# Kernel optimization log

Hardware: AMD Instinct MI355X
Metric: run time of the kernel (lower is better)

Reference implementation:

```python
import jax, jax.numpy as jnp
import numpy as np

D_MODEL = 1024
NUM_HEADS = 16
HEAD_DIM = D_MODEL // NUM_HEADS
THETA = 10000.0
B, S = 4, 2048


def _rope(x, pos):
    # x: [B, H, S, d], pos: [B, S] int
    half = HEAD_DIM // 2
    inv_freq = THETA ** (-(jnp.arange(half, dtype=jnp.float32) * 2.0) / HEAD_DIM)  # [half]
    ang = pos.astype(jnp.float32)[:, None, :, None] * inv_freq  # [B, 1, S, half]
    cos, sin = jnp.cos(ang), jnp.sin(ang)
    x1, x2 = x[..., 0::2], x[..., 1::2]  # interleaved pairs
    r1 = x1 * cos - x2 * sin
    r2 = x1 * sin + x2 * cos
    return jnp.stack([r1, r2], axis=-1).reshape(x.shape)


def setup_inputs() -> dict:
    key = jax.random.key(0)
    ks = jax.random.split(key, 12)
    scale = 1.0 / np.sqrt(D_MODEL)
    inp = {
        "query": jax.random.normal(ks[0], (B, S, D_MODEL), dtype=jnp.float32),
        "key": jax.random.normal(ks[1], (B, S, D_MODEL), dtype=jnp.float32),
        "value": jax.random.normal(ks[2], (B, S, D_MODEL), dtype=jnp.float32),
        "token_positions": jnp.broadcast_to(jnp.arange(S, dtype=jnp.int32), (B, S)),
        "w_q": jax.random.normal(ks[3], (D_MODEL, D_MODEL), dtype=jnp.float32) * scale,
        "b_q": jnp.zeros((D_MODEL,), dtype=jnp.float32),
        "w_k": jax.random.normal(ks[4], (D_MODEL, D_MODEL), dtype=jnp.float32) * scale,
        "b_k": jnp.zeros((D_MODEL,), dtype=jnp.float32),
        "w_v": jax.random.normal(ks[5], (D_MODEL, D_MODEL), dtype=jnp.float32) * scale,
        "b_v": jnp.zeros((D_MODEL,), dtype=jnp.float32),
        "w_o": jax.random.normal(ks[6], (D_MODEL, D_MODEL), dtype=jnp.float32) * scale,
        "b_o": jnp.zeros((D_MODEL,), dtype=jnp.float32),
    }
    return inp


def reference(query, key, value, token_positions, w_q, b_q, w_k, b_k, w_v, b_v, w_o, b_o):
    b, s, _ = query.shape
    Q = query @ w_q + b_q
    K = key @ w_k + b_k
    V = value @ w_v + b_v
    # [B, S, H, d] -> [B, H, S, d]
    Q = Q.reshape(b, s, NUM_HEADS, HEAD_DIM).transpose(0, 2, 1, 3)
    K = K.reshape(b, s, NUM_HEADS, HEAD_DIM).transpose(0, 2, 1, 3)
    V = V.reshape(b, s, NUM_HEADS, HEAD_DIM).transpose(0, 2, 1, 3)
    Q = _rope(Q, token_positions)
    K = _rope(K, token_positions)
    scores = jnp.einsum("bhqd,bhkd->bhqk", Q, K) / jnp.sqrt(jnp.float32(HEAD_DIM))
    causal = jnp.tril(jnp.ones((s, s), dtype=bool))
    scores = jnp.where(causal, scores, -jnp.inf)
    attn = jax.nn.softmax(scores, axis=-1)
    out = jnp.einsum("bhqk,bhkd->bhqd", attn, V)
    out = out.transpose(0, 2, 1, 3).reshape(b, s, D_MODEL)
    return out @ w_o + b_o
```

## Files before the change

kernel.cpp:

```cpp
#include <hip/hip_runtime.h>

typedef __bf16 bf16;
typedef __attribute__((ext_vector_type(8))) __bf16 bf16x8;
typedef __attribute__((ext_vector_type(4))) __bf16 bf16x4;
typedef __attribute__((ext_vector_type(4))) float floatx4;

#define MFMA16(a, b, c) __builtin_amdgcn_mfma_f32_16x16x32_bf16((a), (b), (c), 0, 0, 0)

#define GLL(g, l)                                                   \
  __builtin_amdgcn_global_load_lds(                                 \
      (const __attribute__((address_space(1))) void*)(g),           \
      (__attribute__((address_space(3))) void*)(l), 16, 0, 0)

static constexpr int DM = 1024;
static constexpr int SEQ = 2048;
static constexpr int BATCH = 4;
static constexpr int NH = 16;
static constexpr int HD = 64;
static constexpr float LOG2E = 1.4426950408889634f;
static constexpr float LOG2_THETA = 13.287712379549449f;
static constexpr float QSC = 0.125f * LOG2E;

__global__ __launch_bounds__(256) void convert_x(
    const float* __restrict__ q, const float* __restrict__ k,
    const float* __restrict__ v, bf16* __restrict__ qo,
    bf16* __restrict__ ko, bf16* __restrict__ vo) {
  int z = blockIdx.z;
  const float* src = (z == 0) ? q : (z == 1) ? k : v;
  bf16* dst = (z == 0) ? qo : (z == 1) ? ko : vo;
  size_t i = ((size_t)blockIdx.x * blockDim.x + threadIdx.x) * 8;
  float4 a = *(const float4*)(src + i);
  float4 b = *(const float4*)(src + i + 4);
  bf16x8 o;
  o[0] = (bf16)a.x; o[1] = (bf16)a.y; o[2] = (bf16)a.z; o[3] = (bf16)a.w;
  o[4] = (bf16)b.x; o[5] = (bf16)b.y; o[6] = (bf16)b.z; o[7] = (bf16)b.w;
  *(bf16x8*)(dst + i) = o;
}

__global__ __launch_bounds__(256) void convert_w(
    const float* __restrict__ wq, const float* __restrict__ wk,
    const float* __restrict__ wv, const float* __restrict__ wo,
    bf16* __restrict__ oq, bf16* __restrict__ ok, bf16* __restrict__ ov,
    bf16* __restrict__ oo) {
  int z = blockIdx.z;
  const float* src = (z == 0) ? wq : (z == 1) ? wk : (z == 2) ? wv : wo;
  bf16* dst = (z == 0) ? oq : (z == 1) ? ok : (z == 2) ? ov : oo;
  __shared__ __align__(16) bf16 T[64][72];
  int k0 = blockIdx.y * 64, n0 = blockIdx.x * 64;
  int tid = threadIdx.x;
  int r = tid >> 4, c4 = (tid & 15) * 4;
#pragma unroll
  for (int i = 0; i < 4; i++) {
    int kk = r + i * 16;
    float4 v = *(const float4*)(src + (size_t)(k0 + kk) * DM + n0 + c4);
    T[c4 + 0][kk] = (bf16)v.x;
    T[c4 + 1][kk] = (bf16)v.y;
    T[c4 + 2][kk] = (bf16)v.z;
    T[c4 + 3][kk] = (bf16)v.w;
  }
  __syncthreads();
#pragma unroll
  for (int i = 0; i < 4; i++) {
    int nn = r + i * 16;
    bf16x4 o = *(const bf16x4*)&T[nn][c4];
    *(bf16x4*)(dst + (size_t)(n0 + nn) * DM + k0 + c4) = o;
  }
}

__global__ __launch_bounds__(256) void rope_table(const int* __restrict__ tp,
                                                  float* __restrict__ tab) {
  int idx = blockIdx.x * 256 + threadIdx.x;
  int m = idx >> 5, i = idx & 31;
  float pos = (float)tp[m];
  float invf = exp2f(-(float)(2 * i) * (LOG2_THETA / 64.0f));
  float s, c;
  sincosf(pos * invf, &s, &c);
  tab[(size_t)idx * 2] = c;
  tab[(size_t)idx * 2 + 1] = s;
}

__global__ __launch_bounds__(256) void gemm_qkv(
    const bf16* __restrict__ qb, const bf16* __restrict__ kb,
    const bf16* __restrict__ vb, const bf16* __restrict__ wqt,
    const bf16* __restrict__ wkt, const bf16* __restrict__ wvt,
    const float* __restrict__ biq, const float* __restrict__ bik,
    const float* __restrict__ biv, const float* __restrict__ tab,
    bf16* __restrict__ Qr, bf16* __restrict__ Kr, bf16* __restrict__ Vr) {
  int z = blockIdx.z;
  const bf16* X = (z == 0) ? qb : (z == 1) ? kb : vb;
  const bf16* Wt = (z == 0) ? wqt : (z == 1) ? wkt : wvt;
  const float* bias = (z == 0) ? biq : (z == 1) ? bik : biv;

  __shared__ __align__(16) bf16 As[128 * 32];
  __shared__ __align__(16) bf16 Bs[128 * 32];
  int lin = blockIdx.x;
  int m0 = (lin & 63) * 128, n0 = (lin >> 6) * 128;
  int tid = threadIdx.x;
  int lane = tid & 63, wv = tid >> 6;
  int quad = lane >> 4, low = lane & 15;
  int wm = (wv >> 1) * 64, wn = (wv & 1) * 64;
  int lr = lane >> 2, lc = (lane & 3) * 8;
  const bf16* AgL = X + (size_t)(m0 + wv * 16 + lr) * DM + lc;
  const bf16* BgL = Wt + (size_t)(n0 + wv * 16 + lr) * DM + lc;
  bf16* AsL = As + wv * 512;
  bf16* BsL = Bs + wv * 512;

  floatx4 acc[4][4];
#pragma unroll
  for (int i = 0; i < 4; i++)
#pragma unroll
    for (int j = 0; j < 4; j++) acc[i][j] = (floatx4)0.0f;

  for (int kt = 0; kt < DM; kt += 32) {
    GLL(AgL + kt, AsL);
    GLL(AgL + kt + (size_t)64 * DM, AsL + 2048);
    GLL(BgL + kt, BsL);
    GLL(BgL + kt + (size_t)64 * DM, BsL + 2048);
    __syncthreads();
    bf16x8 xf[4], wf[4];
#pragma unroll
    for (int t = 0; t < 4; t++)
      xf[t] = *(const bf16x8*)&As[(wm + t * 16 + low) * 32 + quad * 8];
#pragma unroll
    for (int t = 0; t < 4; t++)
      wf[t] = *(const bf16x8*)&Bs[(wn + t * 16 + low) * 32 + quad * 8];
#pragma unroll
    for (int i = 0; i < 4; i++)
#pragma unroll
      for (int j = 0; j < 4; j++)
        acc[i][j] = MFMA16(wf[i], xf[j], acc[i][j]);
    __syncthreads();
  }

#pragma unroll
  for (int i = 0; i < 4; i++) {
    int nb = n0 + wn + i * 16 + quad * 4;
    float4 bv = *(const float4*)(bias + nb);
    int h = nb >> 6, dbase = nb & 63;
#pragma unroll
    for (int j = 0; j < 4; j++) {
      int m = m0 + wm + j * 16 + low;
      int bb = m >> 11, ss = m & 2047;
      float v0 = acc[i][j][0] + bv.x;
      float v1 = acc[i][j][1] + bv.y;
      float v2 = acc[i][j][2] + bv.z;
      float v3 = acc[i][j][3] + bv.w;
      size_t off = ((size_t)(bb * NH + h) * SEQ + ss) * HD + dbase;
      bf16x4 pk;
      if (z < 2) {
        float4 cs = *(const float4*)(tab + (size_t)m * 64 + dbase);
        float o0 = v0 * cs.x - v1 * cs.y;
        float o1 = v0 * cs.y + v1 * cs.x;
        float o2 = v2 * cs.z - v3 * cs.w;
        float o3 = v2 * cs.w + v3 * cs.z;
        if (z == 0) { o0 *= QSC; o1 *= QSC; o2 *= QSC; o3 *= QSC; }
        pk[0] = (bf16)o0; pk[1] = (bf16)o1;
        pk[2] = (bf16)o2; pk[3] = (bf16)o3;
        bf16* dst = (z == 0) ? Qr : Kr;
        *(bf16x4*)(dst + off) = pk;
      } else {
        pk[0] = (bf16)v0; pk[1] = (bf16)v1;
        pk[2] = (bf16)v2; pk[3] = (bf16)v3;
        *(bf16x4*)(Vr + off) = pk;
      }
    }
  }
}

__global__ __launch_bounds__(256) void transpose_v(const bf16* __restrict__ Vr,
                                                   bf16* __restrict__ Vt) {
  int bh = blockIdx.y;
  int s0 = blockIdx.x * 64;
  __shared__ __align__(16) bf16 T[64][72];
  int t = threadIdx.x;
  int r = t >> 2, c = (t & 3) * 16;
  const bf16* src = Vr + ((size_t)bh * SEQ + s0 + r) * HD + c;
  bf16x8 a = *(const bf16x8*)src;
  bf16x8 b = *(const bf16x8*)(src + 8);
  *(bf16x8*)&T[r][c] = a;
  *(bf16x8*)&T[r][c + 8] = b;
  __syncthreads();
  bf16* dst = Vt + ((size_t)bh * HD + r) * SEQ + s0 + c;
  bf16x8 o0, o1;
#pragma unroll
  for (int j = 0; j < 8; j++) {
    o0[j] = T[c + j][r];
    o1[j] = T[c + 8 + j][r];
  }
  *(bf16x8*)dst = o0;
  *(bf16x8*)(dst + 8) = o1;
}

__global__ __launch_bounds__(256, 2) void attn_fa(const bf16* __restrict__ Qr,
                                                  const bf16* __restrict__ Kr,
                                                  const bf16* __restrict__ Vt,
                                                  bf16* __restrict__ attn) {
  int lin = blockIdx.x;
  int bh = lin & 63, bx = lin >> 6;
  int tid = threadIdx.x, lane = tid & 63, w = tid >> 6;
  int quad = lane >> 4, low = lane & 15;
  __shared__ __align__(16) bf16 Ks[2][64 * 72];
  __shared__ __align__(16) bf16 Vs[2][64 * 72];
  __shared__ __align__(16) bf16 Pl[4][2][16 * 72];
  const bf16* Qh = Qr + (size_t)bh * SEQ * HD;
  const bf16* Kh = Kr + (size_t)bh * SEQ * HD;
  const bf16* Vh = Vt + (size_t)bh * HD * SEQ;
  int bb = bh >> 4, h = bh & 15;

  int sr = tid >> 2, scol = (tid & 3) * 16;
  const bf16* Kg = Kh + (size_t)sr * HD + scol;
  const bf16* Vg = Vh + (size_t)sr * SEQ + scol;
  int sl = sr * 72 + scol;

  bf16x8 ones;
#pragma unroll
  for (int j = 0; j < 8; j++) ones[j] = (bf16)1.0f;

  for (int pass = 0; pass < 2; pass++) {
    int qi = pass ? bx : (15 - bx);
    int ntiles = 2 * qi + 2;
    int qrow0 = qi * 128 + w * 32;

    bf16x8 aq[2][2];
#pragma unroll
    for (int rt = 0; rt < 2; rt++)
#pragma unroll
      for (int kc = 0; kc < 2; kc++)
        aq[rt][kc] = *(const bf16x8*)(Qh +
                                      (size_t)(qrow0 + rt * 16 + low) * HD +
                                      kc * 32 + quad * 8);

    floatx4 accO[2][4];
    floatx4 lacc[2];
#pragma unroll
    for (int rt = 0; rt < 2; rt++) {
      lacc[rt] = (floatx4)0.0f;
#pragma unroll
      for (int nt = 0; nt < 4; nt++) accO[rt][nt] = (floatx4)0.0f;
    }

    {
      bf16x8 k0 = *(const bf16x8*)(Kg);
      bf16x8 k1 = *(const bf16x8*)(Kg + 8);
      bf16x8 v0 = *(const bf16x8*)(Vg);
      bf16x8 v1 = *(const bf16x8*)(Vg + 8);
      *(bf16x8*)&Ks[0][sl] = k0;
      *(bf16x8*)&Ks[0][sl + 8] = k1;
      *(bf16x8*)&Vs[0][sl] = v0;
      *(bf16x8*)&Vs[0][sl + 8] = v1;
    }
    __syncthreads();

    for (int kt = 0; kt < ntiles; kt++) {
      int cur = kt & 1;
      bf16x8 nk0, nk1, nv0, nv1;
      bool pre = (kt + 1 < ntiles);
      if (pre) {
        const bf16* kg = Kg + (size_t)(kt + 1) * (64 * HD);
        const bf16* vg = Vg + (size_t)(kt + 1) * 64;
        nk0 = *(const bf16x8*)(kg);
        nk1 = *(const bf16x8*)(kg + 8);
        nv0 = *(const bf16x8*)(vg);
        nv1 = *(const bf16x8*)(vg + 8);
      }

      floatx4 s2[2][4];
#pragma unroll
      for (int rt = 0; rt < 2; rt++)
#pragma unroll
        for (int nt = 0; nt < 4; nt++) s2[rt][nt] = (floatx4)0.0f;
#pragma unroll
      for (int nt = 0; nt < 4; nt++) {
        bf16x8 kb0 = *(const bf16x8*)&Ks[cur][(nt * 16 + low) * 72 + quad * 8];
        bf16x8 kb1 =
            *(const bf16x8*)&Ks[cur][(nt * 16 + low) * 72 + 32 + quad * 8];
#pragma unroll
        for (int rt = 0; rt < 2; rt++) {
          s2[rt][nt] = MFMA16(kb0, aq[rt][0], s2[rt][nt]);
          s2[rt][nt] = MFMA16(kb1, aq[rt][1], s2[rt][nt]);
        }
      }
      if (kt >= ntiles - 2) {
#pragma unroll
        for (int nt = 0; nt < 4; nt++)
#pragma unroll
          for (int r = 0; r < 4; r++) {
            int kg_ = kt * 64 + nt * 16 + quad * 4 + r;
#pragma unroll
            for (int rt = 0; rt < 2; rt++) {
              int qg = qrow0 + rt * 16 + low;
              if (kg_ > qg) s2[rt][nt][r] = -INFINITY;
            }
          }
      }
#pragma unroll
      for (int rt = 0; rt < 2; rt++)
#pragma unroll
        for (int nt = 0; nt < 4; nt++) {
          bf16x4 pk;
#pragma unroll
          for (int r = 0; r < 4; r++) pk[r] = (bf16)exp2f(s2[rt][nt][r]);
          *(bf16x4*)&Pl[w][rt][low * 72 + nt * 16 + quad * 4] = pk;
        }
      bf16x8 vb0[4], vb1[4];
#pragma unroll
      for (int nt = 0; nt < 4; nt++) {
        vb0[nt] = *(const bf16x8*)&Vs[cur][(nt * 16 + low) * 72 + quad * 8];
        vb1[nt] =
            *(const bf16x8*)&Vs[cur][(nt * 16 + low) * 72 + 32 + quad * 8];
      }
      asm volatile("s_waitcnt lgkmcnt(0)" ::: "memory");
#pragma unroll
      for (int rt = 0; rt < 2; rt++) {
        bf16x8 ap0 = *(const bf16x8*)&Pl[w][rt][low * 72 + quad * 8];
        bf16x8 ap1 = *(const bf16x8*)&Pl[w][rt][low * 72 + 32 + quad * 8];
#pragma unroll
        for (int nt = 0; nt < 4; nt++) {
          accO[rt][nt] = MFMA16(ap0, vb0[nt], accO[rt][nt]);
          accO[rt][nt] = MFMA16(ap1, vb1[nt], accO[rt][nt]);
        }
        lacc[rt] = MFMA16(ap0, ones, lacc[rt]);
        lacc[rt] = MFMA16(ap1, ones, lacc[rt]);
      }
      if (pre) {
        int nb = cur ^ 1;
        *(bf16x8*)&Ks[nb][sl] = nk0;
        *(bf16x8*)&Ks[nb][sl + 8] = nk1;
        *(bf16x8*)&Vs[nb][sl] = nv0;
        *(bf16x8*)&Vs[nb][sl + 8] = nv1;
      }
      __syncthreads();
    }

#pragma unroll
    for (int rt = 0; rt < 2; rt++)
#pragma unroll
      for (int r = 0; r < 4; r++) {
        float inv = 1.0f / lacc[rt][r];
        int q = qrow0 + rt * 16 + quad * 4 + r;
#pragma unroll
        for (int nt = 0; nt < 4; nt++) {
          float o = accO[rt][nt][r] * inv;
          attn[((size_t)(bb * SEQ + q)) * DM + h * HD + nt * 16 + low] =
              (bf16)o;
        }
      }
  }
}

__global__ __launch_bounds__(256) void gemm_out(const bf16* __restrict__ X,
                                                const bf16* __restrict__ Wt,
                                                const float* __restrict__ bias,
                                                float* __restrict__ out) {
  __shared__ __align__(16) bf16 As[128 * 32];
  __shared__ __align__(16) bf16 Bs[128 * 32];
  int lin = blockIdx.x;
  int m0 = (lin & 63) * 128, n0 = (lin >> 6) * 128;
  int tid = threadIdx.x;
  int lane = tid & 63, wv = tid >> 6;
  int quad = lane >> 4, low = lane & 15;
  int wm = (wv >> 1) * 64, wn = (wv & 1) * 64;
  int lr = lane >> 2, lc = (lane & 3) * 8;
  const bf16* AgL = X + (size_t)(m0 + wv * 16 + lr) * DM + lc;
  const bf16* BgL = Wt + (size_t)(n0 + wv * 16 + lr) * DM + lc;
  bf16* AsL = As + wv * 512;
  bf16* BsL = Bs + wv * 512;

  floatx4 acc[4][4];
#pragma unroll
  for (int i = 0; i < 4; i++)
#pragma unroll
    for (int j = 0; j < 4; j++) acc[i][j] = (floatx4)0.0f;

  for (int kt = 0; kt < DM; kt += 32) {
    GLL(AgL + kt, AsL);
    GLL(AgL + kt + (size_t)64 * DM, AsL + 2048);
    GLL(BgL + kt, BsL);
    GLL(BgL + kt + (size_t)64 * DM, BsL + 2048);
    __syncthreads();
    bf16x8 xf[4], wf[4];
#pragma unroll
    for (int t = 0; t < 4; t++)
      xf[t] = *(const bf16x8*)&As[(wm + t * 16 + low) * 32 + quad * 8];
#pragma unroll
    for (int t = 0; t < 4; t++)
      wf[t] = *(const bf16x8*)&Bs[(wn + t * 16 + low) * 32 + quad * 8];
#pragma unroll
    for (int i = 0; i < 4; i++)
#pragma unroll
      for (int j = 0; j < 4; j++)
        acc[i][j] = MFMA16(wf[i], xf[j], acc[i][j]);
    __syncthreads();
  }

#pragma unroll
  for (int i = 0; i < 4; i++) {
    int nb = n0 + wn + i * 16 + quad * 4;
    float4 bv = *(const float4*)(bias + nb);
#pragma unroll
    for (int j = 0; j < 4; j++) {
      int m = m0 + wm + j * 16 + low;
      float4 o;
      o.x = acc[i][j][0] + bv.x;
      o.y = acc[i][j][1] + bv.y;
      o.z = acc[i][j][2] + bv.z;
      o.w = acc[i][j][3] + bv.w;
      *(float4*)(out + (size_t)m * DM + nb) = o;
    }
  }
}

extern "C" void kernel_launch(void* const* d_in, const int* in_sizes, int n_in,
                              void* d_out, int out_size, void* d_ws,
                              size_t ws_size, hipStream_t stream) {
  const float* query = (const float*)d_in[0];
  const float* key_ = (const float*)d_in[1];
  const float* value = (const float*)d_in[2];
  const int* tp = (const int*)d_in[3];
  const float* w_q = (const float*)d_in[4];
  const float* b_q = (const float*)d_in[5];
  const float* w_k = (const float*)d_in[6];
  const float* b_k = (const float*)d_in[7];
  const float* w_v = (const float*)d_in[8];
  const float* b_v = (const float*)d_in[9];
  const float* w_o = (const float*)d_in[10];
  const float* b_o = (const float*)d_in[11];

  char* w = (char*)d_ws;
  const size_t MB = 1u << 20;
  bf16* qb = (bf16*)(w + 0);
  bf16* kb = (bf16*)(w + 16 * MB);
  bf16* vb = (bf16*)(w + 32 * MB);
  bf16* wqt = (bf16*)(w + 48 * MB);
  bf16* wkt = (bf16*)(w + 50 * MB);
  bf16* wvt = (bf16*)(w + 52 * MB);
  bf16* wot = (bf16*)(w + 54 * MB);
  bf16* Qr = (bf16*)(w + 56 * MB);
  bf16* Kr = (bf16*)(w + 72 * MB);
  bf16* Vr = (bf16*)(w + 88 * MB);
  float* tab = (float*)(w + 104 * MB);
  bf16* Vt = (bf16*)(w + 32 * MB);
  bf16* attnb = (bf16*)(w + 0);

  convert_x<<<dim3(4096, 1, 3), 256, 0, stream>>>(query, key_, value, qb, kb,
                                                  vb);
  convert_w<<<dim3(16, 16, 4), 256, 0, stream>>>(w_q, w_k, w_v, w_o, wqt, wkt,
                                                 wvt, wot);
  rope_table<<<1024, 256, 0, stream>>>(tp, tab);
  gemm_qkv<<<dim3(512, 1, 3), 256, 0, stream>>>(qb, kb, vb, wqt, wkt, wvt,
                                                b_q, b_k, b_v, tab, Qr, Kr,
                                                Vr);
  transpose_v<<<dim3(32, 64), 256, 0, stream>>>(Vr, Vt);
  attn_fa<<<dim3(512), 256, 0, stream>>>(Qr, Kr, Vt, attnb);
  gemm_out<<<dim3(512), 256, 0, stream>>>(attnb, wot, b_o, (float*)d_out);
}
```

Baseline: 353.5 us.

## Widen GEMM K-tile with XOR-swizzled LDS and split attention into one tile per block

Both projection GEMMs now stage a 64-wide K slice per iteration into LDS using an XOR swizzle on the column chunk. This halves the number of barriers per K loop and is meant to avoid LDS bank conflicts on the fragment reads. The attention kernel drops the two-pass pairing of query tiles and launches 1024 blocks, each handling one query tile. It also uses a single P staging buffer per wave and raises the occupancy hint to 3 blocks per CU. The balanced pairing that evened out causal work is lost in favour of more, smaller blocks and higher occupancy.

Result: faster. 334.0 us (-5.5%).

```diff
diff --git a/kernel.cpp b/kernel.cpp
--- a/kernel.cpp
+++ b/kernel.cpp
@@ -91,19 +91,21 @@
   const bf16* Wt = (z == 0) ? wqt : (z == 1) ? wkt : wvt;
   const float* bias = (z == 0) ? biq : (z == 1) ? bik : biv;
 
-  __shared__ __align__(16) bf16 As[128 * 32];
-  __shared__ __align__(16) bf16 Bs[128 * 32];
+  __shared__ __align__(16) bf16 As[128 * 64];
+  __shared__ __align__(16) bf16 Bs[128 * 64];
   int lin = blockIdx.x;
   int m0 = (lin & 63) * 128, n0 = (lin >> 6) * 128;
   int tid = threadIdx.x;
   int lane = tid & 63, wv = tid >> 6;
   int quad = lane >> 4, low = lane & 15;
   int wm = (wv >> 1) * 64, wn = (wv & 1) * 64;
-  int lr = lane >> 2, lc = (lane & 3) * 8;
-  const bf16* AgL = X + (size_t)(m0 + wv * 16 + lr) * DM + lc;
-  const bf16* BgL = Wt + (size_t)(n0 + wv * 16 + lr) * DM + lc;
-  bf16* AsL = As + wv * 512;
-  bf16* BsL = Bs + wv * 512;
+  int lr8 = lane >> 3;
+  int swcol = ((lane & 7) ^ lr8) * 8;
+  const bf16* AgL = X + (size_t)(m0 + wv * 8 + lr8) * DM + swcol;
+  const bf16* BgL = Wt + (size_t)(n0 + wv * 8 + lr8) * DM + swcol;
+  bf16* AsL = As + wv * 8 * 64;
+  bf16* BsL = Bs + wv * 8 * 64;
+  int r3 = low & 7;
 
   floatx4 acc[4][4];
 #pragma unroll
@@ -111,24 +113,30 @@
 #pragma unroll
     for (int j = 0; j < 4; j++) acc[i][j] = (floatx4)0.0f;
 
-  for (int kt = 0; kt < DM; kt += 32) {
-    GLL(AgL + kt, AsL);
-    GLL(AgL + kt + (size_t)64 * DM, AsL + 2048);
-    GLL(BgL + kt, BsL);
-    GLL(BgL + kt + (size_t)64 * DM, BsL + 2048);
+  for (int kt = 0; kt < DM; kt += 64) {
+#pragma unroll
+    for (int c = 0; c < 4; c++) {
+      GLL(AgL + kt + (size_t)(c * 32) * DM, AsL + c * 2048);
+      GLL(BgL + kt + (size_t)(c * 32) * DM, BsL + c * 2048);
+    }
     __syncthreads();
-    bf16x8 xf[4], wf[4];
-#pragma unroll
-    for (int t = 0; t < 4; t++)
-      xf[t] = *(const bf16x8*)&As[(wm + t * 16 + low) * 32 + quad * 8];
-#pragma unroll
-    for (int t = 0; t < 4; t++)
-      wf[t] = *(const bf16x8*)&Bs[(wn + t * 16 + low) * 32 + quad * 8];
-#pragma unroll
-    for (int i = 0; i < 4; i++)
-#pragma unroll
-      for (int j = 0; j < 4; j++)
-        acc[i][j] = MFMA16(wf[i], xf[j], acc[i][j]);
+#pragma unroll
+    for (int kc = 0; kc < 2; kc++) {
+      bf16x8 xf[4], wf[4];
+#pragma unroll
+      for (int t = 0; t < 4; t++)
+        xf[t] = *(const bf16x8*)&As[(wm + t * 16 + low) * 64 +
+                                    (((kc << 2) | quad) ^ r3) * 8];
+#pragma unroll
+      for (int t = 0; t < 4; t++)
+        wf[t] = *(const bf16x8*)&Bs[(wn + t * 16 + low) * 64 +
+                                    (((kc << 2) | quad) ^ r3) * 8];
+#pragma unroll
+      for (int i = 0; i < 4; i++)
+#pragma unroll
+        for (int j = 0; j < 4; j++)
+          acc[i][j] = MFMA16(wf[i], xf[j], acc[i][j]);
+    }
     __syncthreads();
   }
 
@@ -191,21 +199,23 @@
   *(bf16x8*)(dst + 8) = o1;
 }
 
-__global__ __launch_bounds__(256, 2) void attn_fa(const bf16* __restrict__ Qr,
+__global__ __launch_bounds__(256, 3) void attn_fa(const bf16* __restrict__ Qr,
                                                   const bf16* __restrict__ Kr,
                                                   const bf16* __restrict__ Vt,
                                                   bf16* __restrict__ attn) {
   int lin = blockIdx.x;
-  int bh = lin & 63, bx = lin >> 6;
+  int bh = lin & 63, qi = 15 - (lin >> 6);
+  int ntiles = 2 * qi + 2;
   int tid = threadIdx.x, lane = tid & 63, w = tid >> 6;
   int quad = lane >> 4, low = lane & 15;
   __shared__ __align__(16) bf16 Ks[2][64 * 72];
   __shared__ __align__(16) bf16 Vs[2][64 * 72];
-  __shared__ __align__(16) bf16 Pl[4][2][16 * 72];
+  __shared__ __align__(16) bf16 Pl[4][16 * 72];
   const bf16* Qh = Qr + (size_t)bh * SEQ * HD;
   const bf16* Kh = Kr + (size_t)bh * SEQ * HD;
   const bf16* Vh = Vt + (size_t)bh * HD * SEQ;
   int bb = bh >> 4, h = bh & 15;
+  int qrow0 = qi * 128 + w * 32;
 
   int sr = tid >> 2, scol = (tid & 3) * 16;
   const bf16* Kg = Kh + (size_t)sr * HD + scol;
@@ -216,155 +226,150 @@
 #pragma unroll
   for (int j = 0; j < 8; j++) ones[j] = (bf16)1.0f;
 
-  for (int pass = 0; pass < 2; pass++) {
-    int qi = pass ? bx : (15 - bx);
-    int ntiles = 2 * qi + 2;
-    int qrow0 = qi * 128 + w * 32;
-
-    bf16x8 aq[2][2];
+  bf16x8 aq[2][2];
+#pragma unroll
+  for (int rt = 0; rt < 2; rt++)
+#pragma unroll
+    for (int kc = 0; kc < 2; kc++)
+      aq[rt][kc] = *(const bf16x8*)(Qh + (size_t)(qrow0 + rt * 16 + low) * HD +
+                                    kc * 32 + quad * 8);
+
+  floatx4 accO[2][4];
+  floatx4 lacc[2];
+#pragma unroll
+  for (int rt = 0; rt < 2; rt++) {
+    lacc[rt] = (floatx4)0.0f;
+#pragma unroll
+    for (int nt = 0; nt < 4; nt++) accO[rt][nt] = (floatx4)0.0f;
+  }
+
+  {
+    bf16x8 k0 = *(const bf16x8*)(Kg);
+    bf16x8 k1 = *(const bf16x8*)(Kg + 8);
+    bf16x8 v0 = *(const bf16x8*)(Vg);
+    bf16x8 v1 = *(const bf16x8*)(Vg + 8);
+    *(bf16x8*)&Ks[0][sl] = k0;
+    *(bf16x8*)&Ks[0][sl + 8] = k1;
+    *(bf16x8*)&Vs[0][sl] = v0;
+    *(bf16x8*)&Vs[0][sl + 8] = v1;
+  }
+  __syncthreads();
+
+  for (int kt = 0; kt < ntiles; kt++) {
+    int cur = kt & 1;
+    bf16x8 nk0, nk1, nv0, nv1;
+    bool pre = (kt + 1 < ntiles);
+    if (pre) {
+      const bf16* kg = Kg + (size_t)(kt + 1) * (64 * HD);
+      const bf16* vg = Vg + (size_t)(kt + 1) * 64;
+      nk0 = *(const bf16x8*)(kg);
+      nk1 = *(const bf16x8*)(kg + 8);
+      nv0 = *(const bf16x8*)(vg);
+      nv1 = *(const bf16x8*)(vg + 8);
+    }
+
+    floatx4 s2[2][4];
 #pragma unroll
     for (int rt = 0; rt < 2; rt++)
 #pragma unroll
-      for (int kc = 0; kc < 2; kc++)
-        aq[rt][kc] = *(const bf16x8*)(Qh +
-                                      (size_t)(qrow0 + rt * 16 + low) * HD +
-                                      kc * 32 + quad * 8);
-
-    floatx4 accO[2][4];
-    floatx4 lacc[2];
+      for (int nt = 0; nt < 4; nt++) s2[rt][nt] = (floatx4)0.0f;
+#pragma unroll
+    for (int nt = 0; nt < 4; nt++) {
+      bf16x8 kb0 = *(const bf16x8*)&Ks[cur][(nt * 16 + low) * 72 + quad * 8];
+      bf16x8 kb1 =
+          *(const bf16x8*)&Ks[cur][(nt * 16 + low) * 72 + 32 + quad * 8];
+#pragma unroll
+      for (int rt = 0; rt < 2; rt++) {
+        s2[rt][nt] = MFMA16(kb0, aq[rt][0], s2[rt][nt]);
+        s2[rt][nt] = MFMA16(kb1, aq[rt][1], s2[rt][nt]);
+      }
+    }
+    if (kt >= ntiles - 2) {
+#pragma unroll
+      for (int nt = 0; nt < 4; nt++)
+#pragma unroll
+        for (int r = 0; r < 4; r++) {
+          int kg_ = kt * 64 + nt * 16 + quad * 4 + r;
+#pragma unroll
+          for (int rt = 0; rt < 2; rt++) {
+            int qg = qrow0 + rt * 16 + low;
+            if (kg_ > qg) s2[rt][nt][r] = -INFINITY;
+          }
+        }
+    }
+    bf16x4 pk[2][4];
+#pragma unroll
+    for (int rt = 0; rt < 2; rt++)
+#pragma unroll
+      for (int nt = 0; nt < 4; nt++)
+#pragma unroll
+        for (int r = 0; r < 4; r++)
+          pk[rt][nt][r] = (bf16)exp2f(s2[rt][nt][r]);
+    bf16x8 vb0[4], vb1[4];
+#pragma unroll
+    for (int nt = 0; nt < 4; nt++) {
+      vb0[nt] = *(const bf16x8*)&Vs[cur][(nt * 16 + low) * 72 + quad * 8];
+      vb1[nt] = *(const bf16x8*)&Vs[cur][(nt * 16 + low) * 72 + 32 + quad * 8];
+    }
 #pragma unroll
     for (int rt = 0; rt < 2; rt++) {
-      lacc[rt] = (floatx4)0.0f;
-#pragma unroll
-      for (int nt = 0; nt < 4; nt++) accO[rt][nt] = (floatx4)0.0f;
-    }
-
-    {
-      bf16x8 k0 = *(const bf16x8*)(Kg);
-      bf16x8 k1 = *(const bf16x8*)(Kg + 8);
-      bf16x8 v0 = *(const bf16x8*)(Vg);
-      bf16x8 v1 = *(const bf16x8*)(Vg + 8);
-      *(bf16x8*)&Ks[0][sl] = k0;
-      *(bf16x8*)&Ks[0][sl + 8] = k1;
-      *(bf16x8*)&Vs[0][sl] = v0;
-      *(bf16x8*)&Vs[0][sl + 8] = v1;
+#pragma unroll
+      for (int nt = 0; nt < 4; nt++)
+        *(bf16x4*)&Pl[w][low * 72 + nt * 16 + quad * 4] = pk[rt][nt];
+      asm volatile("s_waitcnt lgkmcnt(0)" ::: "memory");
+      bf16x8 ap0 = *(const bf16x8*)&Pl[w][low * 72 + quad * 8];
+      bf16x8 ap1 = *(const bf16x8*)&Pl[w][low * 72 + 32 + quad * 8];
+#pragma unroll
+      for (int nt = 0; nt < 4; nt++) {
+        accO[rt][nt] = MFMA16(ap0, vb0[nt], accO[rt][nt]);
+        accO[rt][nt] = MFMA16(ap1, vb1[nt], accO[rt][nt]);
+      }
+      lacc[rt] = MFMA16(ap0, ones, lacc[rt]);
+      lacc[rt] = MFMA16(ap1, ones, lacc[rt]);
+    }
+    if (pre) {
+      int nb = cur ^ 1;
+      *(bf16x8*)&Ks[nb][sl] = nk0;
+      *(bf16x8*)&Ks[nb][sl + 8] = nk1;
+      *(bf16x8*)&Vs[nb][sl] = nv0;
+      *(bf16x8*)&Vs[nb][sl + 8] = nv1;
     }
     __syncthreads();
-
-    for (int kt = 0; kt < ntiles; kt++) {
-      int cur = kt & 1;
-      bf16x8 nk0, nk1, nv0, nv1;
-      bool pre = (kt + 1 < ntiles);
-      if (pre) {
-        const bf16* kg = Kg + (size_t)(kt + 1) * (64 * HD);
-        const bf16* vg = Vg + (size_t)(kt + 1) * 64;
-        nk0 = *(const bf16x8*)(kg);
-        nk1 = *(const bf16x8*)(kg + 8);
-        nv0 = *(const bf16x8*)(vg);
-        nv1 = *(const bf16x8*)(vg + 8);
+  }
+
+#pragma unroll
+  for (int rt = 0; rt < 2; rt++)
+#pragma unroll
+    for (int r = 0; r < 4; r++) {
+      float inv = 1.0f / lacc[rt][r];
+      int q = qrow0 + rt * 16 + quad * 4 + r;
+#pragma unroll
+      for (int nt = 0; nt < 4; nt++) {
+        float o = accO[rt][nt][r] * inv;
+        attn[((size_t)(bb * SEQ + q)) * DM + h * HD + nt * 16 + low] = (bf16)o;
       }
-
-      floatx4 s2[2][4];
-#pragma unroll
-      for (int rt = 0; rt < 2; rt++)
-#pragma unroll
-        for (int nt = 0; nt < 4; nt++) s2[rt][nt] = (floatx4)0.0f;
-#pragma unroll
-      for (int nt = 0; nt < 4; nt++) {
-        bf16x8 kb0 = *(const bf16x8*)&Ks[cur][(nt * 16 + low) * 72 + quad * 8];
-        bf16x8 kb1 =
-            *(const bf16x8*)&Ks[cur][(nt * 16 + low) * 72 + 32 + quad * 8];
-#pragma unroll
-        for (int rt = 0; rt < 2; rt++) {
-          s2[rt][nt] = MFMA16(kb0, aq[rt][0], s2[rt][nt]);
-          s2[rt][nt] = MFMA16(kb1, aq[rt][1], s2[rt][nt]);
-        }
-      }
-      if (kt >= ntiles - 2) {
-#pragma unroll
-        for (int nt = 0; nt < 4; nt++)
-#pragma unroll
-          for (int r = 0; r < 4; r++) {
-            int kg_ = kt * 64 + nt * 16 + quad * 4 + r;
-#pragma unroll
-            for (int rt = 0; rt < 2; rt++) {
-              int qg = qrow0 + rt * 16 + low;
-              if (kg_ > qg) s2[rt][nt][r] = -INFINITY;
-            }
-          }
-      }
-#pragma unroll
-      for (int rt = 0; rt < 2; rt++)
-#pragma unroll
-        for (int nt = 0; nt < 4; nt++) {
-          bf16x4 pk;
-#pragma unroll
-          for (int r = 0; r < 4; r++) pk[r] = (bf16)exp2f(s2[rt][nt][r]);
-          *(bf16x4*)&Pl[w][rt][low * 72 + nt * 16 + quad * 4] = pk;
-        }
-      bf16x8 vb0[4], vb1[4];
-#pragma unroll
-      for (int nt = 0; nt < 4; nt++) {
-        vb0[nt] = *(const bf16x8*)&Vs[cur][(nt * 16 + low) * 72 + quad * 8];
-        vb1[nt] =
-            *(const bf16x8*)&Vs[cur][(nt * 16 + low) * 72 + 32 + quad * 8];
-      }
-      asm volatile("s_waitcnt lgkmcnt(0)" ::: "memory");
-#pragma unroll
-      for (int rt = 0; rt < 2; rt++) {
-        bf16x8 ap0 = *(const bf16x8*)&Pl[w][rt][low * 72 + quad * 8];
-        bf16x8 ap1 = *(const bf16x8*)&Pl[w][rt][low * 72 + 32 + quad * 8];
-#pragma unroll
-        for (int nt = 0; nt < 4; nt++) {
-          accO[rt][nt] = MFMA16(ap0, vb0[nt], accO[rt][nt]);
-          accO[rt][nt] = MFMA16(ap1, vb1[nt], accO[rt][nt]);
-        }
-        lacc[rt] = MFMA16(ap0, ones, lacc[rt]);
-        lacc[rt] = MFMA16(ap1, ones, lacc[rt]);
-      }
-      if (pre) {
-        int nb = cur ^ 1;
-        *(bf16x8*)&Ks[nb][sl] = nk0;
-        *(bf16x8*)&Ks[nb][sl + 8] = nk1;
-        *(bf16x8*)&Vs[nb][sl] = nv0;
-        *(bf16x8*)&Vs[nb][sl + 8] = nv1;
-      }
-      __syncthreads();
-    }
-
-#pragma unroll
-    for (int rt = 0; rt < 2; rt++)
-#pragma unroll
-      for (int r = 0; r < 4; r++) {
-        float inv = 1.0f / lacc[rt][r];
-        int q = qrow0 + rt * 16 + quad * 4 + r;
-#pragma unroll
-        for (int nt = 0; nt < 4; nt++) {
-          float o = accO[rt][nt][r] * inv;
-          attn[((size_t)(bb * SEQ + q)) * DM + h * HD + nt * 16 + low] =
-              (bf16)o;
-        }
-      }
-  }
+    }
 }
 
 __global__ __launch_bounds__(256) void gemm_out(const bf16* __restrict__ X,
                                                 const bf16* __restrict__ Wt,
                                                 const float* __restrict__ bias,
                                                 float* __restrict__ out) {
-  __shared__ __align__(16) bf16 As[128 * 32];
-  __shared__ __align__(16) bf16 Bs[128 * 32];
+  __shared__ __align__(16) bf16 As[128 * 64];
+  __shared__ __align__(16) bf16 Bs[128 * 64];
   int lin = blockIdx.x;
   int m0 = (lin & 63) * 128, n0 = (lin >> 6) * 128;
   int tid = threadIdx.x;
   int lane = tid & 63, wv = tid >> 6;
   int quad = lane >> 4, low = lane & 15;
   int wm = (wv >> 1) * 64, wn = (wv & 1) * 64;
-  int lr = lane >> 2, lc = (lane & 3) * 8;
-  const bf16* AgL = X + (size_t)(m0 + wv * 16 + lr) * DM + lc;
-  const bf16* BgL = Wt + (size_t)(n0 + wv * 16 + lr) * DM + lc;
-  bf16* AsL = As + wv * 512;
-  bf16* BsL = Bs + wv * 512;
+  int lr8 = lane >> 3;
+  int swcol = ((lane & 7) ^ lr8) * 8;
+  const bf16* AgL = X + (size_t)(m0 + wv * 8 + lr8) * DM + swcol;
+  const bf16* BgL = Wt + (size_t)(n0 + wv * 8 + lr8) * DM + swcol;
+  bf16* AsL = As + wv * 8 * 64;
+  bf16* BsL = Bs + wv * 8 * 64;
+  int r3 = low & 7;
 
   floatx4 acc[4][4];
 #pragma unroll
@@ -372,24 +377,30 @@
 #pragma unroll
     for (int j = 0; j < 4; j++) acc[i][j] = (floatx4)0.0f;
 
-  for (int kt = 0; kt < DM; kt += 32) {
-    GLL(AgL + kt, AsL);
-    GLL(AgL + kt + (size_t)64 * DM, AsL + 2048);
-    GLL(BgL + kt, BsL);
-    GLL(BgL + kt + (size_t)64 * DM, BsL + 2048);
+  for (int kt = 0; kt < DM; kt += 64) {
+#pragma unroll
+    for (int c = 0; c < 4; c++) {
+      GLL(AgL + kt + (size_t)(c * 32) * DM, AsL + c * 2048);
+      GLL(BgL + kt + (size_t)(c * 32) * DM, BsL + c * 2048);
+    }
     __syncthreads();
-    bf16x8 xf[4], wf[4];
-#pragma unroll
-    for (int t = 0; t < 4; t++)
-      xf[t] = *(const bf16x8*)&As[(wm + t * 16 + low) * 32 + quad * 8];
-#pragma unroll
-    for (int t = 0; t < 4; t++)
-      wf[t] = *(const bf16x8*)&Bs[(wn + t * 16 + low) * 32 + quad * 8];
-#pragma unroll
-    for (int i = 0; i < 4; i++)
-#pragma unroll
-      for (int j = 0; j < 4; j++)
-        acc[i][j] = MFMA16(wf[i], xf[j], acc[i][j]);
+#pragma unroll
+    for (int kc = 0; kc < 2; kc++) {
+      bf16x8 xf[4], wf[4];
+#pragma unroll
+      for (int t = 0; t < 4; t++)
+        xf[t] = *(const bf16x8*)&As[(wm + t * 16 + low) * 64 +
+                                    (((kc << 2) | quad) ^ r3) * 8];
+#pragma unroll
+      for (int t = 0; t < 4; t++)
+        wf[t] = *(const bf16x8*)&Bs[(wn + t * 16 + low) * 64 +
+                                    (((kc << 2) | quad) ^ r3) * 8];
+#pragma unroll
+      for (int i = 0; i < 4; i++)
+#pragma unroll
+        for (int j = 0; j < 4; j++)
+          acc[i][j] = MFMA16(wf[i], xf[j], acc[i][j]);
+    }
     __syncthreads();
   }
 
@@ -451,6 +462,6 @@
                                                 b_q, b_k, b_v, tab, Qr, Kr,
                                                 Vr);
   transpose_v<<<dim3(32, 64), 256, 0, stream>>>(Vr, Vt);
-  attn_fa<<<dim3(512), 256, 0, stream>>>(Qr, Kr, Vt, attnb);
+  attn_fa<<<dim3(1024), 256, 0, stream>>>(Qr, Kr, Vt, attnb);
   gemm_out<<<dim3(512), 256, 0, stream>>>(attnb, wot, b_o, (float*)d_out);
 }
```
